# Optimization experiments

Hardware: AMD Instinct MI355X
Metric: run time of the kernel (lower is better)

Reference implementation:

```python
import jax, jax.numpy as jnp
import numpy as np

HEADS = 4
DIM_HEAD = 128


def setup_inputs() -> dict:
    key = jax.random.key(0)
    k1, k2, k3 = jax.random.split(key, 3)
    dim = 256
    hidden = HEADS * DIM_HEAD  # 512
    x = jax.random.normal(k1, (16, dim, 64, 64), dtype=jnp.float32)
    # 1x1 conv weights stored as [out_ch, in_ch] (kernel dims squeezed)
    w_qkv = jax.random.normal(k2, (hidden * 3, dim), dtype=jnp.float32) * (1.0 / np.sqrt(dim))
    w_out = jax.random.normal(k3, (dim, hidden), dtype=jnp.float32) * (1.0 / np.sqrt(hidden))
    b_out = jnp.zeros((dim,), dtype=jnp.float32)
    return {"x": x, "w_qkv": w_qkv, "w_out": w_out, "b_out": b_out}


def reference(x, w_qkv, w_out, b_out):
    b, c, h, w = x.shape
    n = h * w
    # 1x1 conv == per-pixel linear projection
    qkv = jnp.einsum('bchw,oc->bohw', x, w_qkv)           # [b, 3*heads*dh, h, w]
    qkv = qkv.reshape(b, 3, HEADS, DIM_HEAD, n)           # 'b (qkv heads c) h w -> qkv b heads c (h w)'
    q, k, v = qkv[:, 0], qkv[:, 1], qkv[:, 2]             # [b, heads, dh, n]
    k = jax.nn.softmax(k, axis=-1)                        # softmax over spatial positions
    context = jnp.einsum('bhdn,bhen->bhde', k, v)         # [b, heads, dh, dh]
    out = jnp.einsum('bhde,bhdn->bhen', context, q)       # [b, heads, dh, n]
    out = out.reshape(b, HEADS * DIM_HEAD, h, w)          # 'b heads c (h w) -> b (heads c) h w'
    y = jnp.einsum('bchw,oc->bohw', out, w_out) + b_out[None, :, None, None]
    return y
```

## Files before the change

kernel.cpp:

```cpp
#include <hip/hip_runtime.h>

#define BATCH 16
#define CIN   256
#define NSP   4096
#define HID   512

typedef short v8s __attribute__((ext_vector_type(8)));
typedef float v4f __attribute__((ext_vector_type(4)));

__device__ __forceinline__ unsigned short f2bf(float f) {
    union { float f; unsigned u; } a; a.f = f;
    unsigned r = a.u + 0x7fffu + ((a.u >> 16) & 1u);
    return (unsigned short)(r >> 16);
}

__device__ __forceinline__ void gld_lds16(const unsigned short* g, unsigned short* l) {
    __builtin_amdgcn_global_load_lds(
        (const __attribute__((address_space(1))) unsigned int*)g,
        (__attribute__((address_space(3))) unsigned int*)l,
        16, 0, 0);
}


__global__ __launch_bounds__(256) void k_prep(const float* __restrict__ x,
                                              const float* __restrict__ wq,
                                              unsigned short* __restrict__ xbf,
                                              unsigned short* __restrict__ xT,
                                              unsigned short* __restrict__ wbf,
                                              unsigned short* __restrict__ wqT,
                                              float* __restrict__ zacc) {
    const int bid = blockIdx.x;
    const int t = threadIdx.x;
    if (bid >= 4320) {
        zacc[(bid - 4320) * 256 + t] = 0.f;
        return;
    }
    if (bid >= 4096) {
        const int wid = bid - 4096;
        if (wid < 192) {
            const int g = wid * 256 + t;
            const float4 f0 = *(const float4*)(wq + (size_t)g * 8);
            const float4 f1 = *(const float4*)(wq + (size_t)g * 8 + 4);
            union { unsigned short s[8]; uint4 u; } p;
            p.s[0] = f2bf(f0.x); p.s[1] = f2bf(f0.y); p.s[2] = f2bf(f0.z); p.s[3] = f2bf(f0.w);
            p.s[4] = f2bf(f1.x); p.s[5] = f2bf(f1.y); p.s[6] = f2bf(f1.z); p.s[7] = f2bf(f1.w);
            *(uint4*)(wbf + (size_t)g * 8) = p.u;
            return;
        }
        __shared__ float tile[64 * 65];
        const int bb = wid - 192;
        const int u0 = (bb & 7) * 64, c0 = (bb >> 3) * 64;
        {
            const int cl = (t & 15) * 4, ul = t >> 4;
            #pragma unroll
            for (int i = 0; i < 4; i++) {
                int u = ul + i * 16;
                const float4 f = *(const float4*)(wq + (size_t)(u0 + u) * CIN + c0 + cl);
                *(float4*)(&tile[u * 65 + cl]) = f;
            }
        }
        __syncthreads();
        {
            const int ul4 = (t & 15) * 4, cl = t >> 4;
            #pragma unroll
            for (int i = 0; i < 4; i++) {
                int c = cl + i * 16;
                union { unsigned short s[4]; uint2 u; } p;
                #pragma unroll
                for (int j = 0; j < 4; j++)
                    p.s[j] = f2bf(tile[(ul4 + j) * 65 + c]);
                *(uint2*)(wqT + (size_t)(c0 + c) * HID + u0 + ul4) = p.u;
            }
        }
        return;
    }
    __shared__ float tile[64 * 65];
    const int n0 = (bid & 63) * 64, c0 = ((bid >> 6) & 3) * 64, bz = bid >> 8;
    const float* xb = x + (size_t)bz * CIN * NSP;
    {
        const int nl = (t & 15) * 4, cl = t >> 4;
        #pragma unroll
        for (int i = 0; i < 4; i++) {
            int c = cl + i * 16;
            const float4 f = *(const float4*)(xb + (size_t)(c0 + c) * NSP + n0 + nl);
            *(float4*)(&tile[c * 65 + nl]) = f;
            union { unsigned short s[4]; uint2 u; } p;
            p.s[0] = f2bf(f.x); p.s[1] = f2bf(f.y); p.s[2] = f2bf(f.z); p.s[3] = f2bf(f.w);
            *(uint2*)(xbf + ((size_t)bz * CIN + c0 + c) * NSP + n0 + nl) = p.u;
        }
    }
    __syncthreads();
    {
        const int cl4 = (t & 15) * 4, nl = t >> 4;
        #pragma unroll
        for (int i = 0; i < 4; i++) {
            int n = nl + i * 16;
            union { unsigned short s[4]; uint2 u; } p;
            #pragma unroll
            for (int j = 0; j < 4; j++)
                p.s[j] = f2bf(tile[(cl4 + j) * 65 + n]);
            *(uint2*)(xT + ((size_t)bz * NSP + n0 + n) * CIN + c0 + cl4) = p.u;
        }
    }
}

__global__ __launch_bounds__(512, 2) void k_ks(const unsigned short* __restrict__ wbf,
                                               const unsigned short* __restrict__ xT,
                                               const unsigned short* __restrict__ xbf,
                                               float* __restrict__ Sp,
                                               float* __restrict__ zacc) {
    __shared__ __align__(16) unsigned short A1s[2][2][128][64];
    __shared__ __align__(16) unsigned short A2s[2][256][64];
    __shared__ __align__(16) unsigned short Es[128 * 128];

    const int t = threadIdx.x;
    const int id = blockIdx.x;
    const int bz = id & 15, dblk = (id >> 4) & 3, nc = id >> 6;
    const int d0 = dblk * 128;
    const int nbase = nc * 1024;
    const int lane = t & 63, wv = t >> 6, quad = lane >> 4, l15 = lane & 15;
    const int srow8 = lane >> 3, sslot = lane & 7;
    const int scol = ((sslot - srow8) & 7) * 8;
    const int sw0 = ((quad + l15) & 7) * 8;
    const int wn = wv & 1, wd1 = wv >> 1;
    const int wc = wv & 3, wd2 = wv >> 2;

    auto STAGE_A1 = [&](int half, int nrow0) {
        #pragma unroll
        for (int i = 0; i < 4; i++) {
            const int flat = wv * 4 + i;
            const int kl = flat >> 4, rb = flat & 15;
            gld_lds16(xT + ((size_t)bz * NSP + nrow0 + rb * 8 + srow8) * CIN + (half * 2 + kl) * 64 + scol,
                      &A1s[half][kl][rb * 8][0]);
        }
    };
    auto STAGE_A2 = [&](int n0s) {
        #pragma unroll
        for (int i = 0; i < 8; i++) {
            const int flat = wv * 8 + i;
            const int kst = flat >> 5, rb = flat & 31;
            gld_lds16(xbf + ((size_t)bz * CIN + rb * 8 + srow8) * NSP + n0s + kst * 64 + scol,
                      &A2s[kst][rb * 8][0]);
        }
    };

    {
        #pragma unroll
        for (int i = 0; i < 8; i++) {
            const int flat = wv * 8 + i;
            const int kk = flat >> 4, rb = flat & 15;
            gld_lds16(wbf + (size_t)(512 + d0 + rb * 8 + srow8) * CIN + kk * 64 + scol,
                      &A2s[0][0][0] + (kk * 128 + rb * 8) * 64);
        }
    }
    __syncthreads();
    v8s Wkf[4][2][2];
    #pragma unroll
    for (int kk = 0; kk < 4; kk++)
        #pragma unroll
        for (int ni = 0; ni < 2; ni++)
            #pragma unroll
            for (int h = 0; h < 2; h++) {
                union { v8s v; uint4 u; } rr;
                rr.u = *(const uint4*)(&A2s[0][0][0] +
                        (size_t)(kk * 128 + wd1 * 32 + ni * 16 + l15) * 64 + (sw0 ^ (h * 32)));
                Wkf[kk][ni][h] = rr.v;
            }
    __syncthreads();

    v4f acc2[4][4];
    #pragma unroll
    for (int i = 0; i < 4; i++)
        #pragma unroll
        for (int j = 0; j < 4; j++) acc2[i][j] = (v4f)0.f;
    float za[2] = {0.f, 0.f};

    STAGE_A1(0, nbase);
    STAGE_A1(1, nbase);

    for (int nt = 0; nt < 8; nt++) {
        const int n0s = nbase + nt * 128;
        __syncthreads();
        STAGE_A2(n0s);

        v4f acc1[4][2];
        #pragma unroll
        for (int i = 0; i < 4; i++)
            #pragma unroll
            for (int j = 0; j < 2; j++) acc1[i][j] = (v4f)0.f;

        __builtin_amdgcn_s_setprio(1);
        #pragma unroll
        for (int kk = 0; kk < 4; kk++) {
            #pragma unroll
            for (int h = 0; h < 2; h++) {
                v8s af[4];
                #pragma unroll
                for (int mi = 0; mi < 4; mi++) {
                    union { v8s v; uint4 u; } rr;
                    rr.u = *(const uint4*)(&A1s[kk >> 1][kk & 1][wn * 64 + mi * 16 + l15][0] + (sw0 ^ (h * 32)));
                    af[mi] = rr.v;
                }
                #pragma unroll
                for (int mi = 0; mi < 4; mi++)
                    #pragma unroll
                    for (int ni = 0; ni < 2; ni++)
                        acc1[mi][ni] = __builtin_amdgcn_mfma_f32_16x16x32_bf16(af[mi], Wkf[kk][ni][h], acc1[mi][ni], 0, 0, 0);
            }
        }
        __builtin_amdgcn_s_setprio(0);

        #pragma unroll
        for (int ni = 0; ni < 2; ni++) {
            const int d = wd1 * 32 + ni * 16 + l15;
            #pragma unroll
            for (int mi = 0; mi < 4; mi++) {
                union { unsigned short s[4]; uint2 u; } p;
                #pragma unroll
                for (int rr = 0; rr < 4; rr++) {
                    float e = __expf(acc1[mi][ni][rr]);
                    za[ni] += e;
                    p.s[rr] = f2bf(e);
                }
                const int slot = (mi * 2 + (quad >> 1) + d) & 7;
                *(uint2*)(&Es[d * 128 + wn * 64 + slot * 8 + (quad & 1) * 4]) = p.u;
            }
        }
        __syncthreads();
        if (nt < 7) {
            STAGE_A1(0, n0s + 128);
            STAGE_A1(1, n0s + 128);
        }

        __builtin_amdgcn_s_setprio(1);
        #pragma unroll
        for (int kst = 0; kst < 2; kst++) {
            #pragma unroll
            for (int h = 0; h < 2; h++) {
                v8s af[4], bfr[4];
                #pragma unroll
                for (int mi = 0; mi < 4; mi++) {
                    union { v8s v; uint4 u; } rr;
                    rr.u = *(const uint4*)(&A2s[kst][wc * 64 + mi * 16 + l15][0] + (sw0 ^ (h * 32)));
                    af[mi] = rr.v;
                }
                #pragma unroll
                for (int ni = 0; ni < 4; ni++) {
                    union { v8s v; uint4 u; } rr;
                    rr.u = *(const uint4*)(&Es[(wd2 * 64 + ni * 16 + l15) * 128 + kst * 64 + (sw0 ^ (h * 32))]);
                    bfr[ni] = rr.v;
                }
                #pragma unroll
                for (int mi = 0; mi < 4; mi++)
                    #pragma unroll
                    for (int ni = 0; ni < 4; ni++)
                        acc2[mi][ni] = __builtin_amdgcn_mfma_f32_16x16x32_bf16(af[mi], bfr[ni], acc2[mi][ni], 0, 0, 0);
            }
        }
        __builtin_amdgcn_s_setprio(0);
    }

    #pragma unroll
    for (int ni = 0; ni < 2; ni++) {
        float z = za[ni];
        z += __shfl_xor(z, 16);
        z += __shfl_xor(z, 32);
        if (quad == 0)
            atomicAdd(&zacc[bz * 512 + d0 + wd1 * 32 + ni * 16 + l15], z);
    }

    const int ch = wc >> 1;
    float* outp = Sp + ((size_t)((bz * 4 + dblk) * 2 + ch) * 4 + nc) * 16384;
    #pragma unroll
    for (int ni = 0; ni < 4; ni++) {
        const int dl = wd2 * 64 + ni * 16 + l15;
        #pragma unroll
        for (int mi = 0; mi < 4; mi++) {
            const int cl = (wc & 1) * 64 + mi * 16 + quad * 4;
            *(v4f*)(outp + dl * 128 + cl) = acc2[mi][ni];
        }
    }
}

__global__ __launch_bounds__(256) void k_sred(const float* __restrict__ Sp,
                                              unsigned short* __restrict__ Sred) {
    const int qv = blockIdx.x * 256 + threadIdx.x;
    const int bh = qv >> 13, r = qv & 8191;
    const int dl = r >> 6, cq6 = r & 63;
    const int ch = cq6 >> 5, clq = cq6 & 31;
    const float* p = Sp + ((size_t)(bh * 2 + ch) * 4) * 16384 + dl * 128 + clq * 4;
    float4 s = *(const float4*)p;
    #pragma unroll
    for (int kc = 1; kc < 4; kc++) {
        const float4 f = *(const float4*)(p + (size_t)kc * 16384);
        s.x += f.x; s.y += f.y; s.z += f.z; s.w += f.w;
    }
    union { unsigned short us[4]; uint2 u; } pk;
    pk.us[0] = f2bf(s.x); pk.us[1] = f2bf(s.y); pk.us[2] = f2bf(s.z); pk.us[3] = f2bf(s.w);
    *(uint2*)(Sred + (size_t)bh * 32768 + dl * 256 + cq6 * 4) = pk.u;
}

__global__ __launch_bounds__(256) void k_redwc(const unsigned short* __restrict__ Sred,
                                               const float* __restrict__ zacc,
                                               const unsigned short* __restrict__ wbf,
                                               const float* __restrict__ w_out,
                                               unsigned short* __restrict__ Wc) {
    __shared__ unsigned short Ds[128 * 136];
    __shared__ float zinv[128];
    const int t = threadIdx.x;
    const int bh = blockIdx.x;  const int b = bh >> 2, h = bh & 3;
    const int lane = t & 63, wv = t >> 6, quad = lane >> 4, l15 = lane & 15;

    if (t < 128) zinv[t] = 1.0f / zacc[b * 512 + h * 128 + t];
    __syncthreads();

    {
        const int wm = (wv & 1) * 64, wn = (wv >> 1) * 64;
        const unsigned short* Sb = Sred + (size_t)bh * 32768;
        const unsigned short* Vb = wbf + (size_t)(1024 + h * 128) * CIN;
        v4f acc[4][4];
        #pragma unroll
        for (int i = 0; i < 4; i++)
            #pragma unroll
            for (int j = 0; j < 4; j++) acc[i][j] = (v4f)0.f;
        for (int kk = 0; kk < CIN; kk += 32) {
            v8s af[4], bfr[4];
            #pragma unroll
            for (int mi = 0; mi < 4; mi++) {
                union { v8s v; uint4 u; } rr;
                rr.u = *(const uint4*)(Sb + (size_t)(wm + mi * 16 + l15) * 256 + kk + quad * 8);
                af[mi] = rr.v;
            }
            #pragma unroll
            for (int ni = 0; ni < 4; ni++) {
                union { v8s v; uint4 u; } rr;
                rr.u = *(const uint4*)(Vb + (size_t)(wn + ni * 16 + l15) * 256 + kk + quad * 8);
                bfr[ni] = rr.v;
            }
            #pragma unroll
            for (int mi = 0; mi < 4; mi++)
                #pragma unroll
                for (int ni = 0; ni < 4; ni++)
                    acc[mi][ni] = __builtin_amdgcn_mfma_f32_16x16x32_bf16(af[mi], bfr[ni], acc[mi][ni], 0, 0, 0);
        }
        float zq[4][4];
        #pragma unroll
        for (int mi = 0; mi < 4; mi++)
            #pragma unroll
            for (int rr = 0; rr < 4; rr++)
                zq[mi][rr] = zinv[wm + mi * 16 + quad * 4 + rr];
        #pragma unroll
        for (int mi = 0; mi < 4; mi++)
            #pragma unroll
            for (int ni = 0; ni < 4; ni++)
                #pragma unroll
                for (int rr = 0; rr < 4; rr++)
                    Ds[(wm + mi * 16 + quad * 4 + rr) * 136 + wn + ni * 16 + l15] =
                        f2bf(acc[mi][ni][rr] * zq[mi][rr]);
    }
    __syncthreads();

    {
        const int wm = wv * 64;
        v4f acc[4][8];
        #pragma unroll
        for (int i = 0; i < 4; i++)
            #pragma unroll
            for (int j = 0; j < 8; j++) acc[i][j] = (v4f)0.f;
        for (int kk = 0; kk < 128; kk += 32) {
            v8s af[4], bfr[8];
            #pragma unroll
            for (int mi = 0; mi < 4; mi++) {
                int o = wm + mi * 16 + l15;
                const float* wp = w_out + (size_t)o * HID + h * 128 + kk + quad * 8;
                float4 f0 = *(const float4*)wp;
                float4 f1 = *(const float4*)(wp + 4);
                union { v8s v; unsigned short s[8]; } r;
                r.s[0] = f2bf(f0.x); r.s[1] = f2bf(f0.y); r.s[2] = f2bf(f0.z); r.s[3] = f2bf(f0.w);
                r.s[4] = f2bf(f1.x); r.s[5] = f2bf(f1.y); r.s[6] = f2bf(f1.z); r.s[7] = f2bf(f1.w);
                af[mi] = r.v;
            }
            #pragma unroll
            for (int ni = 0; ni < 8; ni++) {
                union { v8s v; uint4 u; } r;
                r.u = *(const uint4*)(&Ds[(ni * 16 + l15) * 136 + kk + quad * 8]);
                bfr[ni] = r.v;
            }
            #pragma unroll
            for (int mi = 0; mi < 4; mi++)
                #pragma unroll
                for (int ni = 0; ni < 8; ni++)
                    acc[mi][ni] = __builtin_amdgcn_mfma_f32_16x16x32_bf16(af[mi], bfr[ni], acc[mi][ni], 0, 0, 0);
        }
        #pragma unroll
        for (int ni = 0; ni < 8; ni++) {
            int d = ni * 16 + l15;
            #pragma unroll
            for (int mi = 0; mi < 4; mi++)
                #pragma unroll
                for (int rr = 0; rr < 4; rr++) {
                    int o = wm + mi * 16 + quad * 4 + rr;
                    Wc[((size_t)b * 256 + o) * HID + h * 128 + d] = f2bf(acc[mi][ni][rr]);
                }
        }
    }
}

__global__ __launch_bounds__(256) void k_chain(const unsigned short* __restrict__ Wc,
                                               const unsigned short* __restrict__ wqT,
                                               unsigned short* __restrict__ Weff) {
    __shared__ __align__(16) unsigned short As[128 * 64];
    __shared__ __align__(16) unsigned short Bs[128 * 64];
    const int t = threadIdx.x;
    const int c0 = blockIdx.x * 128, o0 = blockIdx.y * 128, bz = blockIdx.z;
    const int lane = t & 63, wv = t >> 6, quad = lane >> 4, l15 = lane & 15;
    const int wmC = (wv & 1) * 64, wnO = (wv >> 1) * 64;

    const int srow8 = lane >> 3, sslot = lane & 7;
    const int scol = ((sslot - srow8) & 7) * 8;
    const int sw0 = ((quad + l15) & 7) * 8;

    const unsigned short* Ag = wqT + (size_t)(c0 + wv * 32 + srow8) * HID + scol;
    const unsigned short* Bg = Wc + ((size_t)bz * 256 + o0 + wv * 32 + srow8) * HID + scol;
    unsigned short* Al = As + wv * 32 * 64;
    unsigned short* Bl = Bs + wv * 32 * 64;

    v4f acc[4][4];
    #pragma unroll
    for (int i = 0; i < 4; i++)
        #pragma unroll
        for (int j = 0; j < 4; j++) acc[i][j] = (v4f)0.f;

    for (int kk = 0; kk < HID; kk += 64) {
        #pragma unroll
        for (int cc = 0; cc < 4; cc++) {
            gld_lds16(Ag + (size_t)(cc * 8) * HID + kk, Al + cc * 8 * 64);
            gld_lds16(Bg + (size_t)(cc * 8) * HID + kk, Bl + cc * 8 * 64);
        }
        __syncthreads();
        #pragma unroll
        for (int h = 0; h < 2; h++) {
            const int sw = sw0 ^ (h * 32);
            v8s af[4], bfr[4];
            #pragma unroll
            for (int mi = 0; mi < 4; mi++) {
                union { v8s v; uint4 u; } rr;
                rr.u = *(const uint4*)(&As[(wmC + mi * 16 + l15) * 64 + sw]);
                af[mi] = rr.v;
            }
            #pragma unroll
            for (int ni = 0; ni < 4; ni++) {
                union { v8s v; uint4 u; } rr;
                rr.u = *(const uint4*)(&Bs[(wnO + ni * 16 + l15) * 64 + sw]);
                bfr[ni] = rr.v;
            }
            #pragma unroll
            for (int mi = 0; mi < 4; mi++)
                #pragma unroll
                for (int ni = 0; ni < 4; ni++)
                    acc[mi][ni] = __builtin_amdgcn_mfma_f32_16x16x32_bf16(af[mi], bfr[ni], acc[mi][ni], 0, 0, 0);
        }
        __syncthreads();
    }
    #pragma unroll
    for (int ni = 0; ni < 4; ni++) {
        const int o = o0 + wnO + ni * 16 + l15;
        #pragma unroll
        for (int mi = 0; mi < 4; mi++) {
            const int c = c0 + wmC + mi * 16 + quad * 4;
            union { unsigned short s[4]; uint2 u; } p;
            #pragma unroll
            for (int rr = 0; rr < 4; rr++) p.s[rr] = f2bf(acc[mi][ni][rr]);
            *(uint2*)(Weff + ((size_t)bz * 256 + o) * 256 + c) = p.u;
        }
    }
}

__global__ __launch_bounds__(256) void k_y(const unsigned short* __restrict__ Weff,
                                           const unsigned short* __restrict__ xT,
                                           const float* __restrict__ b_out,
                                           float* __restrict__ y) {
    __shared__ __align__(16) unsigned short As[128 * 64];
    __shared__ __align__(16) unsigned short Bs[128 * 64];
    const int t = threadIdx.x;
    const int o0 = blockIdx.x * 128;
    const int n0 = blockIdx.y * 128;
    const int bz = blockIdx.z;
    const int lane = t & 63, wv = t >> 6, quad = lane >> 4, l15 = lane & 15;
    const int wmN = (wv & 1) * 64, wnO = (wv >> 1) * 64;

    const int srow8 = lane >> 3, sslot = lane & 7;
    const int scol = ((sslot - srow8) & 7) * 8;
    const int sw0 = ((quad + l15) & 7) * 8;

    const unsigned short* Ag = xT + ((size_t)bz * NSP + n0 + wv * 32 + srow8) * CIN + scol;
    const unsigned short* Bg = Weff + ((size_t)bz * 256 + o0 + wv * 32 + srow8) * CIN + scol;
    unsigned short* Al = As + wv * 32 * 64;
    unsigned short* Bl = Bs + wv * 32 * 64;

    v4f acc[4][4];
    #pragma unroll
    for (int i = 0; i < 4; i++)
        #pragma unroll
        for (int j = 0; j < 4; j++) acc[i][j] = (v4f)0.f;

    for (int kk = 0; kk < CIN; kk += 64) {
        #pragma unroll
        for (int cc = 0; cc < 4; cc++) {
            gld_lds16(Ag + (size_t)(cc * 8) * CIN + kk, Al + cc * 8 * 64);
            gld_lds16(Bg + (size_t)(cc * 8) * CIN + kk, Bl + cc * 8 * 64);
        }
        __syncthreads();
        #pragma unroll
        for (int h = 0; h < 2; h++) {
            const int sw = sw0 ^ (h * 32);
            v8s af[4], bfr[4];
            #pragma unroll
            for (int mi = 0; mi < 4; mi++) {
                union { v8s v; uint4 u; } rr;
                rr.u = *(const uint4*)(&As[(wmN + mi * 16 + l15) * 64 + sw]);
                af[mi] = rr.v;
            }
            #pragma unroll
            for (int ni = 0; ni < 4; ni++) {
                union { v8s v; uint4 u; } rr;
                rr.u = *(const uint4*)(&Bs[(wnO + ni * 16 + l15) * 64 + sw]);
                bfr[ni] = rr.v;
            }
            #pragma unroll
            for (int mi = 0; mi < 4; mi++)
                #pragma unroll
                for (int ni = 0; ni < 4; ni++)
                    acc[mi][ni] = __builtin_amdgcn_mfma_f32_16x16x32_bf16(af[mi], bfr[ni], acc[mi][ni], 0, 0, 0);
        }
        __syncthreads();
    }
    #pragma unroll
    for (int ni = 0; ni < 4; ni++) {
        const int o = o0 + wnO + ni * 16 + l15;
        const float bias = b_out[o];
        #pragma unroll
        for (int mi = 0; mi < 4; mi++) {
            const int n = n0 + wmN + mi * 16 + quad * 4;
            v4f v = acc[mi][ni];
            v[0] += bias; v[1] += bias; v[2] += bias; v[3] += bias;
            *(v4f*)(y + ((size_t)bz * 256 + o) * NSP + n) = v;
        }
    }
}

extern "C" void kernel_launch(void* const* d_in, const int* in_sizes, int n_in,
                              void* d_out, int out_size, void* d_ws, size_t ws_size,
                              hipStream_t stream) {
    (void)in_sizes; (void)n_in; (void)out_size; (void)ws_size;
    const float* x     = (const float*)d_in[0];
    const float* w_qkv = (const float*)d_in[1];
    const float* w_out = (const float*)d_in[2];
    const float* b_out = (const float*)d_in[3];
    float* y = (float*)d_out;
    char* ws = (char*)d_ws;

    unsigned short* xT   = (unsigned short*)(ws);
    unsigned short* xbf  = (unsigned short*)(ws + 33554432);
    float*          Sp   = (float*)(ws + 134217728);
    float*          zacc = (float*)(ws + 167772160);
    unsigned short* Sred = (unsigned short*)(ws + 167804928);
    unsigned short* Wc   = (unsigned short*)(ws + 171999232);
    unsigned short* Weff = (unsigned short*)(ws + 176193536);
    unsigned short* wbf  = (unsigned short*)(ws + 178290688);
    unsigned short* wqT  = (unsigned short*)(ws + 179077120);

    k_prep <<<dim3(4352),       256, 0, stream>>>(x, w_qkv, xbf, xT, wbf, wqT, zacc);
    k_ks   <<<dim3(256),        512, 0, stream>>>(wbf, xT, xbf, Sp, zacc);
    k_sred <<<dim3(2048),       256, 0, stream>>>(Sp, Sred);
    k_redwc<<<dim3(64),         256, 0, stream>>>(Sred, zacc, wbf, w_out, Wc);
    k_chain<<<dim3(2, 2, 16),   256, 0, stream>>>(Wc, wqT, Weff);
    k_y    <<<dim3(2, 32, 16),  256, 0, stream>>>(Weff, xT, b_out, y);
}
```

Measured before the change: 230.7 us.

## Split k_ks into smaller 256-thread blocks over 64-row key tiles

The k_ks kernel is re-tiled so each block handles 64 key channels instead of 128, uses 256 threads, and walks 16 spatial tiles of 64 instead of 8 of 128. The grid doubles to 512 blocks and shared memory per block shrinks, aiming for better CU occupancy and load balance across the GPU. In exchange, each block re-streams the same x tiles (xT and xbf) for half as many output rows, doubling global traffic for the activations, and there are more barriers per unit of work.

```diff
diff --git a/kernel.cpp b/kernel.cpp
--- a/kernel.cpp
+++ b/kernel.cpp
@@ -104,43 +104,42 @@
     }
 }
 
-__global__ __launch_bounds__(512, 2) void k_ks(const unsigned short* __restrict__ wbf,
+__global__ __launch_bounds__(256, 2) void k_ks(const unsigned short* __restrict__ wbf,
                                                const unsigned short* __restrict__ xT,
                                                const unsigned short* __restrict__ xbf,
                                                float* __restrict__ Sp,
                                                float* __restrict__ zacc) {
-    __shared__ __align__(16) unsigned short A1s[2][2][128][64];
-    __shared__ __align__(16) unsigned short A2s[2][256][64];
-    __shared__ __align__(16) unsigned short Es[128 * 128];
+    __shared__ __align__(16) unsigned short A1s[4][64][64];
+    __shared__ __align__(16) unsigned short A2s[256][64];
+    __shared__ __align__(16) unsigned short Es[64][64];
 
     const int t = threadIdx.x;
     const int id = blockIdx.x;
-    const int bz = id & 15, dblk = (id >> 4) & 3, nc = id >> 6;
-    const int d0 = dblk * 128;
+    const int bz = id & 15, dblk = (id >> 4) & 7, nc = id >> 7;
+    const int d0 = dblk * 64;
     const int nbase = nc * 1024;
     const int lane = t & 63, wv = t >> 6, quad = lane >> 4, l15 = lane & 15;
     const int srow8 = lane >> 3, sslot = lane & 7;
     const int scol = ((sslot - srow8) & 7) * 8;
     const int sw0 = ((quad + l15) & 7) * 8;
     const int wn = wv & 1, wd1 = wv >> 1;
-    const int wc = wv & 3, wd2 = wv >> 2;
-
-    auto STAGE_A1 = [&](int half, int nrow0) {
-        #pragma unroll
-        for (int i = 0; i < 4; i++) {
-            const int flat = wv * 4 + i;
-            const int kl = flat >> 4, rb = flat & 15;
-            gld_lds16(xT + ((size_t)bz * NSP + nrow0 + rb * 8 + srow8) * CIN + (half * 2 + kl) * 64 + scol,
-                      &A1s[half][kl][rb * 8][0]);
+    const int wc = wv;
+
+    auto STAGE_A1 = [&](int n0s) {
+        #pragma unroll
+        for (int i = 0; i < 8; i++) {
+            const int flat = wv * 8 + i;
+            const int kl = flat >> 3, rb = flat & 7;
+            gld_lds16(xT + ((size_t)bz * NSP + n0s + rb * 8 + srow8) * CIN + kl * 64 + scol,
+                      &A1s[kl][rb * 8][0]);
         }
     };
     auto STAGE_A2 = [&](int n0s) {
         #pragma unroll
         for (int i = 0; i < 8; i++) {
-            const int flat = wv * 8 + i;
-            const int kst = flat >> 5, rb = flat & 31;
-            gld_lds16(xbf + ((size_t)bz * CIN + rb * 8 + srow8) * NSP + n0s + kst * 64 + scol,
-                      &A2s[kst][rb * 8][0]);
+            const int rb = wv * 8 + i;
+            gld_lds16(xbf + ((size_t)bz * CIN + rb * 8 + srow8) * NSP + n0s + scol,
+                      &A2s[rb * 8][0]);
         }
     };
 
@@ -148,9 +147,9 @@
         #pragma unroll
         for (int i = 0; i < 8; i++) {
             const int flat = wv * 8 + i;
-            const int kk = flat >> 4, rb = flat & 15;
+            const int kk = flat >> 3, rb = flat & 7;
             gld_lds16(wbf + (size_t)(512 + d0 + rb * 8 + srow8) * CIN + kk * 64 + scol,
-                      &A2s[0][0][0] + (kk * 128 + rb * 8) * 64);
+                      &A2s[0][0] + (kk * 64 + rb * 8) * 64);
         }
     }
     __syncthreads();
@@ -162,8 +161,8 @@
             #pragma unroll
             for (int h = 0; h < 2; h++) {
                 union { v8s v; uint4 u; } rr;
-                rr.u = *(const uint4*)(&A2s[0][0][0] +
-                        (size_t)(kk * 128 + wd1 * 32 + ni * 16 + l15) * 64 + (sw0 ^ (h * 32)));
+                rr.u = *(const uint4*)(&A2s[0][0] +
+                        (size_t)(kk * 64 + wd1 * 32 + ni * 16 + l15) * 64 + (sw0 ^ (h * 32)));
                 Wkf[kk][ni][h] = rr.v;
             }
     __syncthreads();
@@ -175,17 +174,16 @@
         for (int j = 0; j < 4; j++) acc2[i][j] = (v4f)0.f;
     float za[2] = {0.f, 0.f};
 
-    STAGE_A1(0, nbase);
-    STAGE_A1(1, nbase);
-
-    for (int nt = 0; nt < 8; nt++) {
-        const int n0s = nbase + nt * 128;
+    STAGE_A1(nbase);
+
+    for (int nt = 0; nt < 16; nt++) {
+        const int n0s = nbase + nt * 64;
         __syncthreads();
         STAGE_A2(n0s);
 
-        v4f acc1[4][2];
-        #pragma unroll
-        for (int i = 0; i < 4; i++)
+        v4f acc1[2][2];
+        #pragma unroll
+        for (int i = 0; i < 2; i++)
             #pragma unroll
             for (int j = 0; j < 2; j++) acc1[i][j] = (v4f)0.f;
 
@@ -194,15 +192,15 @@
         for (int kk = 0; kk < 4; kk++) {
             #pragma unroll
             for (int h = 0; h < 2; h++) {
-                v8s af[4];
-                #pragma unroll
-                for (int mi = 0; mi < 4; mi++) {
+                v8s af[2];
+                #pragma unroll
+                for (int mi = 0; mi < 2; mi++) {
                     union { v8s v; uint4 u; } rr;
-                    rr.u = *(const uint4*)(&A1s[kk >> 1][kk & 1][wn * 64 + mi * 16 + l15][0] + (sw0 ^ (h * 32)));
+                    rr.u = *(const uint4*)(&A1s[kk][wn * 32 + mi * 16 + l15][0] + (sw0 ^ (h * 32)));
                     af[mi] = rr.v;
                 }
                 #pragma unroll
-                for (int mi = 0; mi < 4; mi++)
+                for (int mi = 0; mi < 2; mi++)
                     #pragma unroll
                     for (int ni = 0; ni < 2; ni++)
                         acc1[mi][ni] = __builtin_amdgcn_mfma_f32_16x16x32_bf16(af[mi], Wkf[kk][ni][h], acc1[mi][ni], 0, 0, 0);
@@ -214,7 +212,7 @@
         for (int ni = 0; ni < 2; ni++) {
             const int d = wd1 * 32 + ni * 16 + l15;
             #pragma unroll
-            for (int mi = 0; mi < 4; mi++) {
+            for (int mi = 0; mi < 2; mi++) {
                 union { unsigned short s[4]; uint2 u; } p;
                 #pragma unroll
                 for (int rr = 0; rr < 4; rr++) {
@@ -222,40 +220,35 @@
                     za[ni] += e;
                     p.s[rr] = f2bf(e);
                 }
-                const int slot = (mi * 2 + (quad >> 1) + d) & 7;
-                *(uint2*)(&Es[d * 128 + wn * 64 + slot * 8 + (quad & 1) * 4]) = p.u;
-            }
-        }
-        __syncthreads();
-        if (nt < 7) {
-            STAGE_A1(0, n0s + 128);
-            STAGE_A1(1, n0s + 128);
-        }
+                const int slot = (wn * 4 + mi * 2 + (quad >> 1) + d) & 7;
+                *(uint2*)(&Es[d][slot * 8 + (quad & 1) * 4]) = p.u;
+            }
+        }
+        __syncthreads();
+        if (nt < 15) STAGE_A1(n0s + 64);
 
         __builtin_amdgcn_s_setprio(1);
         #pragma unroll
         for (int kst = 0; kst < 2; kst++) {
-            #pragma unroll
-            for (int h = 0; h < 2; h++) {
-                v8s af[4], bfr[4];
-                #pragma unroll
-                for (int mi = 0; mi < 4; mi++) {
-                    union { v8s v; uint4 u; } rr;
-                    rr.u = *(const uint4*)(&A2s[kst][wc * 64 + mi * 16 + l15][0] + (sw0 ^ (h * 32)));
-                    af[mi] = rr.v;
-                }
-                #pragma unroll
-                for (int ni = 0; ni < 4; ni++) {
-                    union { v8s v; uint4 u; } rr;
-                    rr.u = *(const uint4*)(&Es[(wd2 * 64 + ni * 16 + l15) * 128 + kst * 64 + (sw0 ^ (h * 32))]);
-                    bfr[ni] = rr.v;
-                }
-                #pragma unroll
-                for (int mi = 0; mi < 4; mi++)
-                    #pragma unroll
-                    for (int ni = 0; ni < 4; ni++)
-                        acc2[mi][ni] = __builtin_amdgcn_mfma_f32_16x16x32_bf16(af[mi], bfr[ni], acc2[mi][ni], 0, 0, 0);
-            }
+            const int esw = sw0 ^ (kst * 32);
+            v8s af[4], bfr[4];
+            #pragma unroll
+            for (int mi = 0; mi < 4; mi++) {
+                union { v8s v; uint4 u; } rr;
+                rr.u = *(const uint4*)(&A2s[wc * 64 + mi * 16 + l15][0] + esw);
+                af[mi] = rr.v;
+            }
+            #pragma unroll
+            for (int ni = 0; ni < 4; ni++) {
+                union { v8s v; uint4 u; } rr;
+                rr.u = *(const uint4*)(&Es[ni * 16 + l15][0] + esw);
+                bfr[ni] = rr.v;
+            }
+            #pragma unroll
+            for (int mi = 0; mi < 4; mi++)
+                #pragma unroll
+                for (int ni = 0; ni < 4; ni++)
+                    acc2[mi][ni] = __builtin_amdgcn_mfma_f32_16x16x32_bf16(af[mi], bfr[ni], acc2[mi][ni], 0, 0, 0);
         }
         __builtin_amdgcn_s_setprio(0);
     }
@@ -269,11 +262,12 @@
             atomicAdd(&zacc[bz * 512 + d0 + wd1 * 32 + ni * 16 + l15], z);
     }
 
+    const int bh = bz * 4 + (dblk >> 1);
     const int ch = wc >> 1;
-    float* outp = Sp + ((size_t)((bz * 4 + dblk) * 2 + ch) * 4 + nc) * 16384;
+    float* outp = Sp + ((size_t)(bh * 2 + ch) * 4 + nc) * 16384;
     #pragma unroll
     for (int ni = 0; ni < 4; ni++) {
-        const int dl = wd2 * 64 + ni * 16 + l15;
+        const int dl = (dblk & 1) * 64 + ni * 16 + l15;
         #pragma unroll
         for (int mi = 0; mi < 4; mi++) {
             const int cl = (wc & 1) * 64 + mi * 16 + quad * 4;
@@ -571,7 +565,7 @@
     unsigned short* wqT  = (unsigned short*)(ws + 179077120);
 
     k_prep <<<dim3(4352),       256, 0, stream>>>(x, w_qkv, xbf, xT, wbf, wqT, zacc);
-    k_ks   <<<dim3(256),        512, 0, stream>>>(wbf, xT, xbf, Sp, zacc);
+    k_ks   <<<dim3(512),        256, 0, stream>>>(wbf, xT, xbf, Sp, zacc);
     k_sred <<<dim3(2048),       256, 0, stream>>>(Sp, Sred);
     k_redwc<<<dim3(64),         256, 0, stream>>>(Sred, zacc, wbf, w_out, Wc);
     k_chain<<<dim3(2, 2, 16),   256, 0, stream>>>(Wc, wqT, Weff);
```

New measurement: 226.4 us. No clear change (-1.8%).
